# Optimization experiments

Measured on AMD Instinct MI355X. Metric: run time of the kernel, lower is better.

The kernel has to match this reference:

```python
import jax, jax.numpy as jnp
import numpy as np

N_NODES = 100000


def _gcn_aggregate(x, edge_index):
    """Symmetric-normalized GCN aggregation with self-loops (PyG gcn_norm).
    Returns A_hat @ x where A_hat = D^-1/2 (A + I) D^-1/2.
    """
    n = x.shape[0]
    row, col = edge_index[0], edge_index[1]          # messages flow row -> col
    loop = jnp.arange(n, dtype=edge_index.dtype)
    src = jnp.concatenate([row, loop])
    dst = jnp.concatenate([col, loop])
    # degree at target nodes (includes self-loop weight 1)
    deg = jax.ops.segment_sum(jnp.ones(src.shape[0], x.dtype), dst, num_segments=n)
    dinv = jnp.where(deg > 0, jax.lax.rsqrt(deg), 0.0)
    coef = dinv[src] * dinv[dst]                     # [E+N]
    msg = x[src] * coef[:, None]                     # [E+N, F] gather + scale
    return jax.ops.segment_sum(msg, dst, num_segments=n)  # [N, F] scatter-add


def setup_inputs() -> dict:
    key = jax.random.key(0)
    k1, k2, k3, k4 = jax.random.split(key, 4)
    in_size, out_size = 128, 64
    n_edges = 3200000
    x = jax.random.normal(k1, (N_NODES, in_size), dtype=jnp.float32)
    edge_index = jax.random.randint(k2, (2, n_edges), 0, N_NODES, dtype=jnp.int32)
    scale = 1.0 / np.sqrt(in_size)
    W_mu = jax.random.normal(k3, (in_size, out_size), dtype=jnp.float32) * scale
    W_logstd = jax.random.normal(k4, (in_size, out_size), dtype=jnp.float32) * scale
    b_mu = jnp.zeros((out_size,), jnp.float32)
    b_logstd = jnp.zeros((out_size,), jnp.float32)
    return {"x": x, "edge_index": edge_index, "W_mu": W_mu, "b_mu": b_mu,
            "W_logstd": W_logstd, "b_logstd": b_logstd}


def reference(x, edge_index, W_mu, b_mu, W_logstd, b_logstd):
    # Both GCNConv branches share the same normalized aggregation; by linearity
    # (A_hat @ x) @ W == A_hat @ (x @ W), so aggregate once and apply each linear.
    agg = _gcn_aggregate(x, edge_index)              # [N, in_size]
    mu = agg @ W_mu + b_mu                           # [N, out_size]
    logstd = agg @ W_logstd + b_logstd               # [N, out_size]
    return (mu, logstd)
```

## Files before the change

### kernel.cpp

```cpp
#include <hip/hip_runtime.h>

#define F_IN 128
#define F_OUT 64
#define TILE 4096
#define CAP 4608

__device__ inline unsigned short f2bf(float f) {
    unsigned int x = __builtin_bit_cast(unsigned int, f);
    unsigned int r = x + 0x7FFFu + ((x >> 16) & 1u);
    return (unsigned short)(r >> 16);
}

__global__ void tile_sort(const int* __restrict__ row, const int* __restrict__ col,
                          int* __restrict__ offT, int* __restrict__ bpacked,
                          int E, int NB, int NT) {
    __shared__ int hist[1024];
    __shared__ int gscan[256];
    __shared__ int cur[1024];
    const int t = threadIdx.x;
    const int tile = blockIdx.x;
    const int base = tile * TILE;
    const int n = min(TILE, E - base);

    for (int i = t; i < 1024; i += 256) hist[i] = 0;
    __syncthreads();
    for (int i = t; i < n; i += 256)
        atomicAdd(&hist[col[base + i] >> 7], 1);
    __syncthreads();

    const int h0 = hist[4 * t + 0];
    const int h1 = hist[4 * t + 1];
    const int h2 = hist[4 * t + 2];
    const int h3 = hist[4 * t + 3];
    const int gsum = h0 + h1 + h2 + h3;
    gscan[t] = gsum;
    __syncthreads();
    int incl = gsum;
    for (int off = 1; off < 256; off <<= 1) {
        int v = (t >= off) ? gscan[t - off] : 0;
        __syncthreads();
        incl += v;
        gscan[t] = incl;
        __syncthreads();
    }
    const int gbase = incl - gsum;
    cur[4 * t + 0] = gbase;
    cur[4 * t + 1] = gbase + h0;
    cur[4 * t + 2] = gbase + h0 + h1;
    cur[4 * t + 3] = gbase + h0 + h1 + h2;
    __syncthreads();

    for (int b = t; b < NB; b += 256)
        offT[(size_t)b * NT + tile] = cur[b];
    if (t == 0) offT[(size_t)NB * NT + tile] = n;
    __syncthreads();

    for (int i = t; i < n; i += 256) {
        const int c = col[base + i];
        const int b = c >> 7;
        const int pos = atomicAdd(&cur[b], 1);
        bpacked[base + pos] = row[base + i] | ((c & 127) << 17);
    }
}

__global__ void build2(const int* __restrict__ offT, const int* __restrict__ bpacked,
                       int* __restrict__ srcs, float* __restrict__ dinv,
                       int2* __restrict__ segs, int N, int NT) {
    const int b = blockIdx.x;
    const int t = threadIdx.x;
    __shared__ int hist[128];
    __shared__ int excl[128];
    __shared__ int cursor[128];
    if (t < 128) hist[t] = 0;
    __syncthreads();
    const int* offRow0 = offT + (size_t)b * NT;
    const int* offRow1 = offT + (size_t)(b + 1) * NT;

    for (int tt = t; tt < NT; tt += 256) {
        const int s = offRow0[tt], e = offRow1[tt];
        const int tb = tt * TILE;
        for (int i = s; i < e; i++)
            atomicAdd(&hist[bpacked[tb + i] >> 17], 1);
    }
    __syncthreads();
    if (t < 128) excl[t] = hist[t];
    __syncthreads();
    for (int off = 1; off < 128; off <<= 1) {
        int v = (t < 128 && t >= off) ? excl[t - off] : 0;
        __syncthreads();
        if (t < 128) excl[t] += v;
        __syncthreads();
    }
    const int sbase = b * CAP;
    if (t < 128) {
        const int ex = min(excl[t] - hist[t], CAP);
        cursor[t] = ex;
        const int node = b * 128 + t;
        if (node < N) {
            dinv[node] = rsqrtf((float)hist[t] + 1.0f);
            const int dg = min(hist[t], CAP - ex);
            segs[node] = make_int2(sbase + ex, dg);
        }
    }
    __syncthreads();
    for (int tt = t; tt < NT; tt += 256) {
        const int s = offRow0[tt], e = offRow1[tt];
        const int tb = tt * TILE;
        for (int i = s; i < e; i++) {
            const int p = bpacked[tb + i];
            const int pos = atomicAdd(&cursor[p >> 17], 1);
            if (pos < CAP) srcs[sbase + pos] = p & 0x1FFFF;
        }
    }
}

__global__ __launch_bounds__(256) void gemm_kernel(
        const float* __restrict__ x, const float* __restrict__ Wmu,
        const float* __restrict__ Wls, const float* __restrict__ dinv,
        unsigned int* __restrict__ y, int N) {
    __shared__ float xs[64 * F_IN];
    const int tid = threadIdx.x;
    const int base = blockIdx.x * 64;
    const int nn = min(64, N - base);
    {
        const float4* xg = (const float4*)(x + (size_t)base * F_IN);
        float4* xs4 = (float4*)xs;
        const int cnt = nn * (F_IN / 4);
        for (int i = tid; i < cnt; i += 256) xs4[i] = xg[i];
    }
    __syncthreads();
    const int wv = tid >> 6;
    const int lane = tid & 63;
    const int half = lane >> 5;
    const int lp = lane & 31;
    const int nbase = wv * 16 + half * 8;
    const float* W0 = (lp < 16) ? Wmu : Wls;
    const int coff = (lp < 16) ? (4 * lp) : (4 * (lp - 16));
    float acc[8][4];
#pragma unroll
    for (int n = 0; n < 8; n++)
#pragma unroll
        for (int c = 0; c < 4; c++) acc[n][c] = 0.f;

    for (int k = 0; k < F_IN; k += 4) {
        const float4 w0 = *(const float4*)&W0[(size_t)(k + 0) * F_OUT + coff];
        const float4 w1 = *(const float4*)&W0[(size_t)(k + 1) * F_OUT + coff];
        const float4 w2 = *(const float4*)&W0[(size_t)(k + 2) * F_OUT + coff];
        const float4 w3 = *(const float4*)&W0[(size_t)(k + 3) * F_OUT + coff];
#pragma unroll
        for (int n = 0; n < 8; n++) {
            const float4 xv = *(const float4*)&xs[(nbase + n) * F_IN + k];
            acc[n][0] = fmaf(xv.x, w0.x, acc[n][0]);
            acc[n][1] = fmaf(xv.x, w0.y, acc[n][1]);
            acc[n][2] = fmaf(xv.x, w0.z, acc[n][2]);
            acc[n][3] = fmaf(xv.x, w0.w, acc[n][3]);
            acc[n][0] = fmaf(xv.y, w1.x, acc[n][0]);
            acc[n][1] = fmaf(xv.y, w1.y, acc[n][1]);
            acc[n][2] = fmaf(xv.y, w1.z, acc[n][2]);
            acc[n][3] = fmaf(xv.y, w1.w, acc[n][3]);
            acc[n][0] = fmaf(xv.z, w2.x, acc[n][0]);
            acc[n][1] = fmaf(xv.z, w2.y, acc[n][1]);
            acc[n][2] = fmaf(xv.z, w2.z, acc[n][2]);
            acc[n][3] = fmaf(xv.z, w2.w, acc[n][3]);
            acc[n][0] = fmaf(xv.w, w3.x, acc[n][0]);
            acc[n][1] = fmaf(xv.w, w3.y, acc[n][1]);
            acc[n][2] = fmaf(xv.w, w3.z, acc[n][2]);
            acc[n][3] = fmaf(xv.w, w3.w, acc[n][3]);
        }
    }
    const int ci = (lp < 16) ? (2 * lp) : (32 + 2 * (lp - 16));
#pragma unroll
    for (int n = 0; n < 8; n++) {
        const int node = base + nbase + n;
        if (node < N) {
            const float dv = dinv[node];
            const unsigned u0 = (unsigned)f2bf(acc[n][0] * dv) |
                                ((unsigned)f2bf(acc[n][1] * dv) << 16);
            const unsigned u1 = (unsigned)f2bf(acc[n][2] * dv) |
                                ((unsigned)f2bf(acc[n][3] * dv) << 16);
            *(uint2*)&y[(size_t)node * 64 + ci] = make_uint2(u0, u1);
        }
    }
}

__global__ void gather_kernel(const int2* __restrict__ segs, const int* __restrict__ srcs,
                              const uint4* __restrict__ Y, const float* __restrict__ dinv,
                              const float* __restrict__ bmu, const float* __restrict__ bls,
                              float* __restrict__ out, int N) {
    const int wid = threadIdx.x >> 6;
    const int lane = threadIdx.x & 63;
    const int c = blockIdx.x * 4 + wid;
    if (c >= N) return;
    const int2 sg = segs[c];
    const int sb = sg.x;
    const int deg = sg.y;
    const int eg = lane >> 4;
    const int q = lane & 15;

    float4 A = make_float4(0.f, 0.f, 0.f, 0.f);
    float4 B = make_float4(0.f, 0.f, 0.f, 0.f);

#define ACC(u)                                                        \
    do {                                                              \
        A.x += __builtin_bit_cast(float, (u).x << 16);                \
        A.y += __builtin_bit_cast(float, (u).x & 0xFFFF0000u);        \
        A.z += __builtin_bit_cast(float, (u).y << 16);                \
        A.w += __builtin_bit_cast(float, (u).y & 0xFFFF0000u);        \
        B.x += __builtin_bit_cast(float, (u).z << 16);                \
        B.y += __builtin_bit_cast(float, (u).z & 0xFFFF0000u);        \
        B.z += __builtin_bit_cast(float, (u).w << 16);                \
        B.w += __builtin_bit_cast(float, (u).w & 0xFFFF0000u);        \
    } while (0)

    int i = 0;
    for (; i + 32 <= deg; i += 32) {
        const int e0 = srcs[sb + i + 0 + eg];
        const int e1 = srcs[sb + i + 4 + eg];
        const int e2 = srcs[sb + i + 8 + eg];
        const int e3 = srcs[sb + i + 12 + eg];
        const int e4 = srcs[sb + i + 16 + eg];
        const int e5 = srcs[sb + i + 20 + eg];
        const int e6 = srcs[sb + i + 24 + eg];
        const int e7 = srcs[sb + i + 28 + eg];
        const uint4 u0 = Y[(size_t)e0 * 16 + q];
        const uint4 u1 = Y[(size_t)e1 * 16 + q];
        const uint4 u2 = Y[(size_t)e2 * 16 + q];
        const uint4 u3 = Y[(size_t)e3 * 16 + q];
        const uint4 u4 = Y[(size_t)e4 * 16 + q];
        const uint4 u5 = Y[(size_t)e5 * 16 + q];
        const uint4 u6 = Y[(size_t)e6 * 16 + q];
        const uint4 u7 = Y[(size_t)e7 * 16 + q];
        ACC(u0); ACC(u1); ACC(u2); ACC(u3);
        ACC(u4); ACC(u5); ACC(u6); ACC(u7);
    }
    for (; i + 16 <= deg; i += 16) {
        const int e0 = srcs[sb + i + 0 + eg];
        const int e1 = srcs[sb + i + 4 + eg];
        const int e2 = srcs[sb + i + 8 + eg];
        const int e3 = srcs[sb + i + 12 + eg];
        const uint4 u0 = Y[(size_t)e0 * 16 + q];
        const uint4 u1 = Y[(size_t)e1 * 16 + q];
        const uint4 u2 = Y[(size_t)e2 * 16 + q];
        const uint4 u3 = Y[(size_t)e3 * 16 + q];
        ACC(u0); ACC(u1); ACC(u2); ACC(u3);
    }
    for (; i < deg; i += 4) {
        if (i + eg < deg) {
            const int e = srcs[sb + i + eg];
            const uint4 u = Y[(size_t)e * 16 + q];
            ACC(u);
        }
    }

    A.x += __shfl_xor(A.x, 16); A.y += __shfl_xor(A.y, 16);
    A.z += __shfl_xor(A.z, 16); A.w += __shfl_xor(A.w, 16);
    B.x += __shfl_xor(B.x, 16); B.y += __shfl_xor(B.y, 16);
    B.z += __shfl_xor(B.z, 16); B.w += __shfl_xor(B.w, 16);
    A.x += __shfl_xor(A.x, 32); A.y += __shfl_xor(A.y, 32);
    A.z += __shfl_xor(A.z, 32); A.w += __shfl_xor(A.w, 32);
    B.x += __shfl_xor(B.x, 32); B.y += __shfl_xor(B.y, 32);
    B.z += __shfl_xor(B.z, 32); B.w += __shfl_xor(B.w, 32);

    {
        const uint4 u = Y[(size_t)c * 16 + q];
        ACC(u);
    }
#undef ACC

    if (lane < 16) {
        const float dv = dinv[c];
        if (q < 8) {
            const float4 b0 = ((const float4*)bmu)[2 * q];
            const float4 b1 = ((const float4*)bmu)[2 * q + 1];
            float* o = out + (size_t)c * F_OUT + q * 8;
            *(float4*)o = make_float4(b0.x + A.x * dv, b0.y + A.y * dv,
                                      b0.z + A.z * dv, b0.w + A.w * dv);
            *(float4*)(o + 4) = make_float4(b1.x + B.x * dv, b1.y + B.y * dv,
                                            b1.z + B.z * dv, b1.w + B.w * dv);
        } else {
            const float4 b0 = ((const float4*)bls)[2 * (q - 8)];
            const float4 b1 = ((const float4*)bls)[2 * (q - 8) + 1];
            float* o = out + (size_t)(N + c) * F_OUT + (q - 8) * 8;
            *(float4*)o = make_float4(b0.x + A.x * dv, b0.y + A.y * dv,
                                      b0.z + A.z * dv, b0.w + A.w * dv);
            *(float4*)(o + 4) = make_float4(b1.x + B.x * dv, b1.y + B.y * dv,
                                            b1.z + B.z * dv, b1.w + B.w * dv);
        }
    }
}

extern "C" void kernel_launch(void* const* d_in, const int* in_sizes, int n_in,
                              void* d_out, int out_size, void* d_ws, size_t ws_size,
                              hipStream_t stream) {
    const float* x   = (const float*)d_in[0];
    const int*   ei  = (const int*)d_in[1];
    const float* Wmu = (const float*)d_in[2];
    const float* bmu = (const float*)d_in[3];
    const float* Wls = (const float*)d_in[4];
    const float* bls = (const float*)d_in[5];
    float* out = (float*)d_out;

    const int N = in_sizes[0] / F_IN;
    const int E = in_sizes[1] / 2;
    const int* row = ei;
    const int* col = ei + E;
    const int NB = (N + 127) >> 7;
    const int NT = (E + TILE - 1) / TILE;

    char* p = (char*)d_ws;
    auto alloc = [&](size_t bytes) {
        char* r = p;
        p += (bytes + 511) & ~(size_t)511;
        return r;
    };
    int*   offT    = (int*)  alloc((size_t)(NB + 1) * NT * 4);
    int*   bpacked = (int*)  alloc((size_t)E * 4);
    int*   srcs    = (int*)  alloc((size_t)NB * CAP * 4);
    int2*  segs    = (int2*) alloc((size_t)N * 8);
    float* dinv    = (float*)alloc((size_t)N * 4);
    unsigned int* y = (unsigned int*)alloc((size_t)N * F_IN * 2);

    tile_sort<<<NT, 256, 0, stream>>>(row, col, offT, bpacked, E, NB, NT);
    build2<<<NB, 256, 0, stream>>>(offT, bpacked, srcs, dinv, segs, N, NT);
    gemm_kernel<<<(N + 63) / 64, 256, 0, stream>>>(x, Wmu, Wls, dinv, y, N);
    gather_kernel<<<(N + 3) / 4, 256, 0, stream>>>(segs, srcs, (const uint4*)y,
                                                   dinv, bmu, bls, out, N);
}
```

Before: 385.9 us.

## Compute degrees with global atomics and flatten build2 bucket scatter via binary search

Tile sort now also counts per-node in-degree with global atomics, so build2 no longer makes a separate histogram pass over its bucket. build2 prefix-sums the per-tile run lengths and lets each thread handle one flattened element, found by binary search, instead of each thread serially walking one tile's run. The tile size is doubled, which halves the number of runs per bucket so the scan fits 512 entries. The 32-wide unrolled gather loop is also dropped. The cost is 3.2M global atomics, an extra memset, and a binary search per element.

```diff
diff --git a/kernel.cpp b/kernel.cpp
--- a/kernel.cpp
+++ b/kernel.cpp
@@ -2,7 +2,7 @@
 
 #define F_IN 128
 #define F_OUT 64
-#define TILE 4096
+#define TILE 8192
 #define CAP 4608
 
 __device__ inline unsigned short f2bf(float f) {
@@ -12,8 +12,8 @@
 }
 
 __global__ void tile_sort(const int* __restrict__ row, const int* __restrict__ col,
-                          int* __restrict__ offT, int* __restrict__ bpacked,
-                          int E, int NB, int NT) {
+                          int* __restrict__ deg, int* __restrict__ offT,
+                          int* __restrict__ bpacked, int E, int NB, int NT) {
     __shared__ int hist[1024];
     __shared__ int gscan[256];
     __shared__ int cur[1024];
@@ -24,8 +24,11 @@
 
     for (int i = t; i < 1024; i += 256) hist[i] = 0;
     __syncthreads();
-    for (int i = t; i < n; i += 256)
-        atomicAdd(&hist[col[base + i] >> 7], 1);
+    for (int i = t; i < n; i += 256) {
+        const int c = col[base + i];
+        atomicAdd(&hist[c >> 7], 1);
+        atomicAdd(&deg[c], 1);
+    }
     __syncthreads();
 
     const int h0 = hist[4 * t + 0];
@@ -64,53 +67,72 @@
 }
 
 __global__ void build2(const int* __restrict__ offT, const int* __restrict__ bpacked,
-                       int* __restrict__ srcs, float* __restrict__ dinv,
-                       int2* __restrict__ segs, int N, int NT) {
+                       const int* __restrict__ deg, int* __restrict__ srcs,
+                       float* __restrict__ dinv, int2* __restrict__ segs,
+                       int N, int NT) {
     const int b = blockIdx.x;
     const int t = threadIdx.x;
-    __shared__ int hist[128];
-    __shared__ int excl[128];
+    __shared__ int rsE[512];
+    __shared__ int rstart[512];
+    __shared__ int gsc[256];
     __shared__ int cursor[128];
-    if (t < 128) hist[t] = 0;
-    __syncthreads();
-    const int* offRow0 = offT + (size_t)b * NT;
-    const int* offRow1 = offT + (size_t)(b + 1) * NT;
-
-    for (int tt = t; tt < NT; tt += 256) {
-        const int s = offRow0[tt], e = offRow1[tt];
-        const int tb = tt * TILE;
-        for (int i = s; i < e; i++)
-            atomicAdd(&hist[bpacked[tb + i] >> 17], 1);
-    }
-    __syncthreads();
-    if (t < 128) excl[t] = hist[t];
+    __shared__ int tot;
+    const int* r0 = offT + (size_t)b * NT;
+    const int* r1 = offT + (size_t)(b + 1) * NT;
+
+    const int i0 = 2 * t, i1 = 2 * t + 1;
+    int s0 = 0, l0 = 0, s1 = 0, l1 = 0;
+    if (i0 < NT) { s0 = r0[i0]; l0 = r1[i0] - s0; }
+    if (i1 < NT) { s1 = r0[i1]; l1 = r1[i1] - s1; }
+    const int ps = l0 + l1;
+    gsc[t] = ps;
+    __syncthreads();
+    int incl = ps;
+    for (int off = 1; off < 256; off <<= 1) {
+        int v = (t >= off) ? gsc[t - off] : 0;
+        __syncthreads();
+        incl += v;
+        gsc[t] = incl;
+        __syncthreads();
+    }
+    const int pbase = incl - ps;
+    if (i0 < NT) { rsE[i0] = pbase;      rstart[i0] = s0; }
+    if (i1 < NT) { rsE[i1] = pbase + l0; rstart[i1] = s1; }
+    if (t == 255) tot = incl;
+    __syncthreads();
+
+    const int node = b * 128 + t;
+    int dv_ = 0;
+    if (t < 128) { dv_ = (node < N) ? deg[node] : 0; gsc[t] = dv_; }
     __syncthreads();
     for (int off = 1; off < 128; off <<= 1) {
-        int v = (t < 128 && t >= off) ? excl[t - off] : 0;
-        __syncthreads();
-        if (t < 128) excl[t] += v;
+        int v = (t < 128 && t >= off) ? gsc[t - off] : 0;
+        __syncthreads();
+        if (t < 128) gsc[t] += v;
         __syncthreads();
     }
     const int sbase = b * CAP;
     if (t < 128) {
-        const int ex = min(excl[t] - hist[t], CAP);
+        const int ex = min(gsc[t] - dv_, CAP);
         cursor[t] = ex;
-        const int node = b * 128 + t;
         if (node < N) {
-            dinv[node] = rsqrtf((float)hist[t] + 1.0f);
-            const int dg = min(hist[t], CAP - ex);
-            segs[node] = make_int2(sbase + ex, dg);
-        }
-    }
-    __syncthreads();
-    for (int tt = t; tt < NT; tt += 256) {
-        const int s = offRow0[tt], e = offRow1[tt];
-        const int tb = tt * TILE;
-        for (int i = s; i < e; i++) {
-            const int p = bpacked[tb + i];
-            const int pos = atomicAdd(&cursor[p >> 17], 1);
-            if (pos < CAP) srcs[sbase + pos] = p & 0x1FFFF;
-        }
+            dinv[node] = rsqrtf((float)dv_ + 1.0f);
+            segs[node] = make_int2(sbase + ex, min(dv_, CAP - ex));
+        }
+    }
+    __syncthreads();
+
+    const int total = tot;
+    for (int idx = t; idx < total; idx += 256) {
+        int lo = 0, hi = NT - 1;
+        while (lo < hi) {
+            const int mid = (lo + hi + 1) >> 1;
+            if (rsE[mid] <= idx) lo = mid; else hi = mid - 1;
+        }
+        const int j = idx - rsE[lo];
+        const int p = bpacked[lo * TILE + rstart[lo] + j];
+        const int pos = atomicAdd(&cursor[p >> 17], 1);
+        if (pos < CAP) srcs[sbase + pos] = p & 0x1FFFF;
     }
 }
 
@@ -213,26 +235,6 @@
     } while (0)
 
     int i = 0;
-    for (; i + 32 <= deg; i += 32) {
-        const int e0 = srcs[sb + i + 0 + eg];
-        const int e1 = srcs[sb + i + 4 + eg];
-        const int e2 = srcs[sb + i + 8 + eg];
-        const int e3 = srcs[sb + i + 12 + eg];
-        const int e4 = srcs[sb + i + 16 + eg];
-        const int e5 = srcs[sb + i + 20 + eg];
-        const int e6 = srcs[sb + i + 24 + eg];
-        const int e7 = srcs[sb + i + 28 + eg];
-        const uint4 u0 = Y[(size_t)e0 * 16 + q];
-        const uint4 u1 = Y[(size_t)e1 * 16 + q];
-        const uint4 u2 = Y[(size_t)e2 * 16 + q];
-        const uint4 u3 = Y[(size_t)e3 * 16 + q];
-        const uint4 u4 = Y[(size_t)e4 * 16 + q];
-        const uint4 u5 = Y[(size_t)e5 * 16 + q];
-        const uint4 u6 = Y[(size_t)e6 * 16 + q];
-        const uint4 u7 = Y[(size_t)e7 * 16 + q];
-        ACC(u0); ACC(u1); ACC(u2); ACC(u3);
-        ACC(u4); ACC(u5); ACC(u6); ACC(u7);
-    }
     for (; i + 16 <= deg; i += 16) {
         const int e0 = srcs[sb + i + 0 + eg];
         const int e1 = srcs[sb + i + 4 + eg];
@@ -313,15 +315,17 @@
         p += (bytes + 511) & ~(size_t)511;
         return r;
     };
+    int*   deg     = (int*)  alloc((size_t)N * 4);
     int*   offT    = (int*)  alloc((size_t)(NB + 1) * NT * 4);
-    int*   bpacked = (int*)  alloc((size_t)E * 4);
+    int*   bpacked = (int*)  alloc((size_t)NT * TILE * 4);
     int*   srcs    = (int*)  alloc((size_t)NB * CAP * 4);
     int2*  segs    = (int2*) alloc((size_t)N * 8);
     float* dinv    = (float*)alloc((size_t)N * 4);
     unsigned int* y = (unsigned int*)alloc((size_t)N * F_IN * 2);
 
-    tile_sort<<<NT, 256, 0, stream>>>(row, col, offT, bpacked, E, NB, NT);
-    build2<<<NB, 256, 0, stream>>>(offT, bpacked, srcs, dinv, segs, N, NT);
+    hipMemsetAsync(deg, 0, (size_t)N * 4, stream);
+    tile_sort<<<NT, 256, 0, stream>>>(row, col, deg, offT, bpacked, E, NB, NT);
+    build2<<<NB, 256, 0, stream>>>(offT, bpacked, deg, srcs, dinv, segs, N, NT);
     gemm_kernel<<<(N + 63) / 64, 256, 0, stream>>>(x, Wmu, Wls, dinv, y, N);
     gather_kernel<<<(N + 3) / 4, 256, 0, stream>>>(segs, srcs, (const uint4*)y,
                                                    dinv, bmu, bls, out, N);
```

Measured after the change: 454.3 us. 1.18x slower.
